# Performance work log

Measured on AMD Instinct MI355X. Metric: run time of the kernel, lower is better.

## Reference

```python
import jax, jax.numpy as jnp
import numpy as np

B, S, D, E = 4, 2048, 512, 32

def setup_inputs() -> dict:
    key = jax.random.key(0)
    k1, k2, k3 = jax.random.split(key, 3)
    x = jax.random.normal(k1, (B, S, D), dtype=jnp.float32)
    # glorot-ish scaling for weights
    gate_w = jax.random.normal(k2, (D, E), dtype=jnp.float32) * (1.0 / np.sqrt(D))
    gate_b = jnp.zeros((E,), dtype=jnp.float32)
    expert_w = jax.random.normal(k3, (E, D, D), dtype=jnp.float32) * (1.0 / np.sqrt(D))
    return {"x": x, "gate_w": gate_w, "gate_b": gate_b, "expert_w": expert_w}

def reference(x, gate_w, gate_b, expert_w):
    # gate_scores: [B,S,E] (context=None -> route on x itself)
    gate = jax.nn.softmax(jnp.einsum('bsd,de->bse', x, gate_w) + gate_b, axis=-1)
    # Dense soft-MoE: sum_e gate[b,s,e] * (x[b,s,:] @ expert_w[e])
    # Single einsum avoids materializing the [B,S,E,D] intermediate.
    out = jnp.einsum('bse,bsd,edf->bsf', gate, x, expert_w)
    return out
```

## Files before the change

### kernel.cpp

```cpp
#include <hip/hip_runtime.h>

#define TOK 8192
#define DIM 512
#define NE  32
#define KTOT (NE * DIM)

#define BM 128
#define BN 128
#define BK 64

typedef float f32x4 __attribute__((ext_vector_type(4)));
typedef short s16x8 __attribute__((ext_vector_type(8)));

typedef const void __attribute__((address_space(1)))* gp1_t;
typedef void __attribute__((address_space(3)))* lp3_t;

__device__ __forceinline__ void gl_lds16(const void* g, void* l) {
    __builtin_amdgcn_global_load_lds((gp1_t)g, (lp3_t)l, 16, 0, 0);
}

__device__ __forceinline__ ushort f2bf(float f) {
    unsigned u = __builtin_bit_cast(unsigned, f);
    unsigned r = (u + 0x7fffu + ((u >> 16) & 1u)) >> 16;
    return (ushort)r;
}

__global__ __launch_bounds__(256) void k_prep(const float* __restrict__ w,
                                              ushort* __restrict__ wt,
                                              const float* __restrict__ x,
                                              const float* __restrict__ gw,
                                              const float* __restrict__ gb,
                                              float* __restrict__ G,
                                              ushort* __restrict__ xb) {
    __shared__ __align__(16) char smem[64 * 65 * 4];
    const int bx = blockIdx.x;
    const int tid = threadIdx.x;
    if (bx < 2048) {
        float (*tile)[65] = (float(*)[65])smem;
        const int e = bx >> 6;
        const int f0 = ((bx >> 3) & 7) * 64;
        const int d0 = (bx & 7) * 64;
        const int tx = tid & 63, ty = tid >> 6;
        const float* we = w + (size_t)e * DIM * DIM;
#pragma unroll
        for (int i = ty; i < 64; i += 4)
            tile[i][tx] = we[(size_t)(d0 + i) * DIM + f0 + tx];
        __syncthreads();
#pragma unroll
        for (int i = ty; i < 64; i += 4)
            wt[(size_t)(f0 + i) * KTOT + e * DIM + d0 + tx] = f2bf(tile[tx][i]);
    } else {
        float* xs = (float*)smem;
        const int t0 = (bx - 2048) * 8;
        const float* xBase = x + (size_t)t0 * DIM;
#pragma unroll
        for (int k = 0; k < 4; ++k) {
            int i4 = (k * 256 + tid) * 4;
            float4 v = *(const float4*)(xBase + i4);
            xs[i4 + 0] = v.x; xs[i4 + 1] = v.y; xs[i4 + 2] = v.z; xs[i4 + 3] = v.w;
            ushort4 o;
            o.x = f2bf(v.x); o.y = f2bf(v.y); o.z = f2bf(v.z); o.w = f2bf(v.w);
            *(ushort4*)(xb + (size_t)t0 * DIM + i4) = o;
        }
        __syncthreads();
        const int tok = tid >> 5;
        const int e = tid & 31;
        float l = gb[e];
        const float* xr = xs + tok * DIM;
#pragma unroll 8
        for (int d = 0; d < DIM; ++d)
            l += xr[d] * gw[d * NE + e];
        float mx = l;
#pragma unroll
        for (int m = 16; m >= 1; m >>= 1) mx = fmaxf(mx, __shfl_xor(mx, m));
        float ex = expf(l - mx);
        float s = ex;
#pragma unroll
        for (int m = 16; m >= 1; m >>= 1) s += __shfl_xor(s, m);
        G[(size_t)(t0 + tok) * NE + e] = ex / s;
    }
}

__global__ __launch_bounds__(512, 2) void k_moe_gemm(const ushort* __restrict__ xb,
                                                     const ushort* __restrict__ wt,
                                                     const float* __restrict__ G,
                                                     float* __restrict__ out0,
                                                     float* __restrict__ out1) {
    __shared__ __align__(16) ushort As[2][BM * BK];
    __shared__ __align__(16) ushort Bs[2][BN * BK];
    __shared__ float Gs[16][BM];

    const int tid = threadIdx.x;
    const int m0 = blockIdx.y * BM;
    const int n0 = blockIdx.x * BN;
    const int e0 = blockIdx.z * 16;
    float* __restrict__ dst = blockIdx.z ? out1 : out0;

    for (int i = tid; i < 16 * BM; i += 512) {
        int e = i >> 7, r = i & 127;
        Gs[e][r] = G[(size_t)(m0 + r) * NE + e0 + e];
    }

    const int lane = tid & 63;
    const int wave = tid >> 6;
    const int wm = (wave & 3) * 32;
    const int wn = (wave >> 2) * 64;
    const int l15 = lane & 15;
    const int q = lane >> 4;
    const int keyR = l15 & 7;

    const int swz0 = ((q) ^ keyR) * 16;
    const int swz1 = ((4 + q) ^ keyR) * 16;
    const int rowA0 = (wm + l15) * 128;
    const int rowA1 = (wm + 16 + l15) * 128;
    const int rowB0 = (wn + l15) * 128;
    const int rowB1 = (wn + 16 + l15) * 128;
    const int rowB2 = (wn + 32 + l15) * 128;
    const int rowB3 = (wn + 48 + l15) * 128;

    const int srow = tid >> 3;
    const int chunk = tid & 7;
    const int scol = ((chunk ^ (srow & 7)) * 8);
    const ushort* aBase = xb + (size_t)(m0 + srow) * DIM + scol;
    const ushort* bBase = wt + (size_t)(n0 + srow) * KTOT + (size_t)e0 * DIM + scol;
    const int ldsOff = tid * 16;

    const f32x4 zv = {0.f, 0.f, 0.f, 0.f};
    f32x4 acc[2][4];
#pragma unroll
    for (int i = 0; i < 2; ++i)
#pragma unroll
        for (int j = 0; j < 4; ++j) acc[i][j] = zv;

    gl_lds16(aBase, (char*)As[0] + ldsOff);
    gl_lds16(aBase + (size_t)64 * DIM, (char*)As[0] + 8192 + ldsOff);
    gl_lds16(bBase, (char*)Bs[0] + ldsOff);
    gl_lds16(bBase + (size_t)64 * KTOT, (char*)Bs[0] + 8192 + ldsOff);
    __syncthreads();

#pragma unroll 1
    for (int kt = 0; kt < 8; ++kt) {
        const char* Ab = (const char*)As[kt & 1];
#pragma unroll 1
        for (int ee = 0; ee < 16; ++ee) {
            const int gn = kt * 16 + ee + 1;
            if (gn < 128) {
                const ushort* bN = bBase + (size_t)(gn & 15) * DIM + (gn >> 4) * BK;
                char* bL = (char*)Bs[gn & 1] + ldsOff;
                gl_lds16(bN, bL);
                gl_lds16(bN + (size_t)64 * KTOT, bL + 8192);
                if (ee == 15) {
                    const ushort* aN = aBase + (kt + 1) * BK;
                    char* aL = (char*)As[(kt + 1) & 1] + ldsOff;
                    gl_lds16(aN, aL);
                    gl_lds16(aN + (size_t)64 * DIM, aL + 8192);
                }
            }

            const char* Bb = (const char*)Bs[ee & 1];
            f32x4 pacc[2][4];
#pragma unroll
            for (int ks = 0; ks < 2; ++ks) {
                const int swz = ks ? swz1 : swz0;
                s16x8 a0 = *(const s16x8*)(Ab + rowA0 + swz);
                s16x8 a1 = *(const s16x8*)(Ab + rowA1 + swz);
                s16x8 b0 = *(const s16x8*)(Bb + rowB0 + swz);
                s16x8 b1 = *(const s16x8*)(Bb + rowB1 + swz);
                s16x8 b2 = *(const s16x8*)(Bb + rowB2 + swz);
                s16x8 b3 = *(const s16x8*)(Bb + rowB3 + swz);
                if (ks == 0) {
                    pacc[0][0] = __builtin_amdgcn_mfma_f32_16x16x32_bf16(a0, b0, zv, 0, 0, 0);
                    pacc[0][1] = __builtin_amdgcn_mfma_f32_16x16x32_bf16(a0, b1, zv, 0, 0, 0);
                    pacc[0][2] = __builtin_amdgcn_mfma_f32_16x16x32_bf16(a0, b2, zv, 0, 0, 0);
                    pacc[0][3] = __builtin_amdgcn_mfma_f32_16x16x32_bf16(a0, b3, zv, 0, 0, 0);
                    pacc[1][0] = __builtin_amdgcn_mfma_f32_16x16x32_bf16(a1, b0, zv, 0, 0, 0);
                    pacc[1][1] = __builtin_amdgcn_mfma_f32_16x16x32_bf16(a1, b1, zv, 0, 0, 0);
                    pacc[1][2] = __builtin_amdgcn_mfma_f32_16x16x32_bf16(a1, b2, zv, 0, 0, 0);
                    pacc[1][3] = __builtin_amdgcn_mfma_f32_16x16x32_bf16(a1, b3, zv, 0, 0, 0);
                } else {
                    pacc[0][0] = __builtin_amdgcn_mfma_f32_16x16x32_bf16(a0, b0, pacc[0][0], 0, 0, 0);
                    pacc[0][1] = __builtin_amdgcn_mfma_f32_16x16x32_bf16(a0, b1, pacc[0][1], 0, 0, 0);
                    pacc[0][2] = __builtin_amdgcn_mfma_f32_16x16x32_bf16(a0, b2, pacc[0][2], 0, 0, 0);
                    pacc[0][3] = __builtin_amdgcn_mfma_f32_16x16x32_bf16(a0, b3, pacc[0][3], 0, 0, 0);
                    pacc[1][0] = __builtin_amdgcn_mfma_f32_16x16x32_bf16(a1, b0, pacc[1][0], 0, 0, 0);
                    pacc[1][1] = __builtin_amdgcn_mfma_f32_16x16x32_bf16(a1, b1, pacc[1][1], 0, 0, 0);
                    pacc[1][2] = __builtin_amdgcn_mfma_f32_16x16x32_bf16(a1, b2, pacc[1][2], 0, 0, 0);
                    pacc[1][3] = __builtin_amdgcn_mfma_f32_16x16x32_bf16(a1, b3, pacc[1][3], 0, 0, 0);
                }
            }

#pragma unroll
            for (int i = 0; i < 2; ++i) {
                const f32x4 gt = *(const f32x4*)&Gs[ee][wm + i * 16 + q * 4];
#pragma unroll
                for (int j = 0; j < 4; ++j) {
                    acc[i][j][0] += gt[0] * pacc[i][j][0];
                    acc[i][j][1] += gt[1] * pacc[i][j][1];
                    acc[i][j][2] += gt[2] * pacc[i][j][2];
                    acc[i][j][3] += gt[3] * pacc[i][j][3];
                }
            }
            __syncthreads();
        }
    }

#pragma unroll
    for (int i = 0; i < 2; ++i) {
        const int tl = m0 + wm + i * 16 + q * 4;
#pragma unroll
        for (int j = 0; j < 4; ++j) {
            const int f = n0 + wn + j * 16 + l15;
            float* p = dst + (size_t)tl * DIM + f;
            p[0 * DIM] = acc[i][j][0];
            p[1 * DIM] = acc[i][j][1];
            p[2 * DIM] = acc[i][j][2];
            p[3 * DIM] = acc[i][j][3];
        }
    }
}

__global__ __launch_bounds__(256) void k_reduce(float* __restrict__ out,
                                                const float* __restrict__ P) {
    int i = (blockIdx.x * 256 + threadIdx.x) * 4;
    float4 a = *(const float4*)(out + i);
    float4 b = *(const float4*)(P + i);
    a.x += b.x; a.y += b.y; a.z += b.z; a.w += b.w;
    *(float4*)(out + i) = a;
}

extern "C" void kernel_launch(void* const* d_in, const int* in_sizes, int n_in,
                              void* d_out, int out_size, void* d_ws, size_t ws_size,
                              hipStream_t stream) {
    const float* x  = (const float*)d_in[0];
    const float* gw = (const float*)d_in[1];
    const float* gb = (const float*)d_in[2];
    const float* w  = (const float*)d_in[3];
    float* out = (float*)d_out;

    char* ws = (char*)d_ws;
    ushort* xb = (ushort*)ws;
    ushort* wt = (ushort*)(ws + (8u << 20));
    float*  G  = (float*)(ws + (24u << 20));
    float*  P  = (float*)(ws + (25u << 20));

    k_prep<<<dim3(2048 + TOK / 8), dim3(256), 0, stream>>>(w, wt, x, gw, gb, G, xb);
    k_moe_gemm<<<dim3(DIM / BN, TOK / BM, 2), dim3(512), 0, stream>>>(xb, wt, G, out, P);
    k_reduce<<<dim3(TOK * DIM / 1024), dim3(256), 0, stream>>>(out, P);
}
```

Measured before the change: 255.7 us.

## Hold A fragments in registers, shrink N tile, transpose gate layout

```diff
diff --git a/kernel.cpp b/kernel.cpp
--- a/kernel.cpp
+++ b/kernel.cpp
@@ -6,7 +6,7 @@
 #define KTOT (NE * DIM)
 
 #define BM 128
-#define BN 128
+#define BN 64
 #define BK 64
 
 typedef float f32x4 __attribute__((ext_vector_type(4)));
@@ -30,7 +30,7 @@
                                               const float* __restrict__ x,
                                               const float* __restrict__ gw,
                                               const float* __restrict__ gb,
-                                              float* __restrict__ G,
+                                              float* __restrict__ G2,
                                               ushort* __restrict__ xb) {
     __shared__ __align__(16) char smem[64 * 65 * 4];
     const int bx = blockIdx.x;
@@ -77,16 +77,15 @@
         float s = ex;
 #pragma unroll
         for (int m = 16; m >= 1; m >>= 1) s += __shfl_xor(s, m);
-        G[(size_t)(t0 + tok) * NE + e] = ex / s;
-    }
-}
-
-__global__ __launch_bounds__(512, 2) void k_moe_gemm(const ushort* __restrict__ xb,
+        G2[(size_t)e * TOK + t0 + tok] = ex / s;
+    }
+}
+
+__global__ __launch_bounds__(256, 4) void k_moe_gemm(const ushort* __restrict__ xb,
                                                      const ushort* __restrict__ wt,
-                                                     const float* __restrict__ G,
+                                                     const float* __restrict__ G2,
                                                      float* __restrict__ out0,
                                                      float* __restrict__ out1) {
-    __shared__ __align__(16) ushort As[2][BM * BK];
     __shared__ __align__(16) ushort Bs[2][BN * BK];
     __shared__ float Gs[16][BM];
 
@@ -96,108 +95,90 @@
     const int e0 = blockIdx.z * 16;
     float* __restrict__ dst = blockIdx.z ? out1 : out0;
 
-    for (int i = tid; i < 16 * BM; i += 512) {
+    for (int i = tid; i < 16 * BM; i += 256) {
         int e = i >> 7, r = i & 127;
-        Gs[e][r] = G[(size_t)(m0 + r) * NE + e0 + e];
+        Gs[e][r] = G2[(size_t)(e0 + e) * TOK + m0 + r];
     }
 
     const int lane = tid & 63;
     const int wave = tid >> 6;
-    const int wm = (wave & 3) * 32;
-    const int wn = (wave >> 2) * 64;
+    const int wm = (wave & 1) * 64;
+    const int wn = (wave >> 1) * 32;
     const int l15 = lane & 15;
     const int q = lane >> 4;
     const int keyR = l15 & 7;
 
-    const int swz0 = ((q) ^ keyR) * 16;
-    const int swz1 = ((4 + q) ^ keyR) * 16;
-    const int rowA0 = (wm + l15) * 128;
-    const int rowA1 = (wm + 16 + l15) * 128;
-    const int rowB0 = (wn + l15) * 128;
-    const int rowB1 = (wn + 16 + l15) * 128;
-    const int rowB2 = (wn + 32 + l15) * 128;
-    const int rowB3 = (wn + 48 + l15) * 128;
+    int rb[2][2];
+#pragma unroll
+    for (int j = 0; j < 2; ++j)
+#pragma unroll
+        for (int ks = 0; ks < 2; ++ks)
+            rb[j][ks] = (wn + j * 16 + l15) * 128 + (((ks * 4 + q) ^ keyR) << 4);
 
     const int srow = tid >> 3;
-    const int chunk = tid & 7;
-    const int scol = ((chunk ^ (srow & 7)) * 8);
-    const ushort* aBase = xb + (size_t)(m0 + srow) * DIM + scol;
+    const int c8 = tid & 7;
+    const int scol = ((c8 ^ (srow & 7)) * 8);
     const ushort* bBase = wt + (size_t)(n0 + srow) * KTOT + (size_t)e0 * DIM + scol;
+    const ushort* bBase2 = bBase + (size_t)32 * KTOT;
     const int ldsOff = tid * 16;
 
+    const ushort* aP[4];
+#pragma unroll
+    for (int i = 0; i < 4; ++i)
+        aP[i] = xb + (size_t)(m0 + wm + i * 16 + l15) * DIM + q * 8;
+
     const f32x4 zv = {0.f, 0.f, 0.f, 0.f};
-    f32x4 acc[2][4];
-#pragma unroll
-    for (int i = 0; i < 2; ++i)
-#pragma unroll
-        for (int j = 0; j < 4; ++j) acc[i][j] = zv;
-
-    gl_lds16(aBase, (char*)As[0] + ldsOff);
-    gl_lds16(aBase + (size_t)64 * DIM, (char*)As[0] + 8192 + ldsOff);
+    f32x4 acc[4][2];
+#pragma unroll
+    for (int i = 0; i < 4; ++i)
+#pragma unroll
+        for (int j = 0; j < 2; ++j) acc[i][j] = zv;
+
     gl_lds16(bBase, (char*)Bs[0] + ldsOff);
-    gl_lds16(bBase + (size_t)64 * KTOT, (char*)Bs[0] + 8192 + ldsOff);
+    gl_lds16(bBase2, (char*)Bs[0] + 4096 + ldsOff);
     __syncthreads();
 
 #pragma unroll 1
     for (int kt = 0; kt < 8; ++kt) {
-        const char* Ab = (const char*)As[kt & 1];
+        s16x8 a[4][2];
+#pragma unroll
+        for (int i = 0; i < 4; ++i) {
+            a[i][0] = *(const s16x8*)(aP[i] + kt * 64);
+            a[i][1] = *(const s16x8*)(aP[i] + kt * 64 + 32);
+        }
+
 #pragma unroll 1
         for (int ee = 0; ee < 16; ++ee) {
-            const int gn = kt * 16 + ee + 1;
-            if (gn < 128) {
+            const int g = kt * 16 + ee;
+            if (g + 1 < 128) {
+                const int gn = g + 1;
                 const ushort* bN = bBase + (size_t)(gn & 15) * DIM + (gn >> 4) * BK;
                 char* bL = (char*)Bs[gn & 1] + ldsOff;
                 gl_lds16(bN, bL);
-                gl_lds16(bN + (size_t)64 * KTOT, bL + 8192);
-                if (ee == 15) {
-                    const ushort* aN = aBase + (kt + 1) * BK;
-                    char* aL = (char*)As[(kt + 1) & 1] + ldsOff;
-                    gl_lds16(aN, aL);
-                    gl_lds16(aN + (size_t)64 * DIM, aL + 8192);
-                }
+                gl_lds16(bN + (size_t)32 * KTOT, bL + 4096);
             }
 
-            const char* Bb = (const char*)Bs[ee & 1];
-            f32x4 pacc[2][4];
-#pragma unroll
-            for (int ks = 0; ks < 2; ++ks) {
-                const int swz = ks ? swz1 : swz0;
-                s16x8 a0 = *(const s16x8*)(Ab + rowA0 + swz);
-                s16x8 a1 = *(const s16x8*)(Ab + rowA1 + swz);
-                s16x8 b0 = *(const s16x8*)(Bb + rowB0 + swz);
-                s16x8 b1 = *(const s16x8*)(Bb + rowB1 + swz);
-                s16x8 b2 = *(const s16x8*)(Bb + rowB2 + swz);
-                s16x8 b3 = *(const s16x8*)(Bb + rowB3 + swz);
-                if (ks == 0) {
-                    pacc[0][0] = __builtin_amdgcn_mfma_f32_16x16x32_bf16(a0, b0, zv, 0, 0, 0);
-                    pacc[0][1] = __builtin_amdgcn_mfma_f32_16x16x32_bf16(a0, b1, zv, 0, 0, 0);
-                    pacc[0][2] = __builtin_amdgcn_mfma_f32_16x16x32_bf16(a0, b2, zv, 0, 0, 0);
-                    pacc[0][3] = __builtin_amdgcn_mfma_f32_16x16x32_bf16(a0, b3, zv, 0, 0, 0);
-                    pacc[1][0] = __builtin_amdgcn_mfma_f32_16x16x32_bf16(a1, b0, zv, 0, 0, 0);
-                    pacc[1][1] = __builtin_amdgcn_mfma_f32_16x16x32_bf16(a1, b1, zv, 0, 0, 0);
-                    pacc[1][2] = __builtin_amdgcn_mfma_f32_16x16x32_bf16(a1, b2, zv, 0, 0, 0);
-                    pacc[1][3] = __builtin_amdgcn_mfma_f32_16x16x32_bf16(a1, b3, zv, 0, 0, 0);
-                } else {
-                    pacc[0][0] = __builtin_amdgcn_mfma_f32_16x16x32_bf16(a0, b0, pacc[0][0], 0, 0, 0);
-                    pacc[0][1] = __builtin_amdgcn_mfma_f32_16x16x32_bf16(a0, b1, pacc[0][1], 0, 0, 0);
-                    pacc[0][2] = __builtin_amdgcn_mfma_f32_16x16x32_bf16(a0, b2, pacc[0][2], 0, 0, 0);
-                    pacc[0][3] = __builtin_amdgcn_mfma_f32_16x16x32_bf16(a0, b3, pacc[0][3], 0, 0, 0);
-                    pacc[1][0] = __builtin_amdgcn_mfma_f32_16x16x32_bf16(a1, b0, pacc[1][0], 0, 0, 0);
-                    pacc[1][1] = __builtin_amdgcn_mfma_f32_16x16x32_bf16(a1, b1, pacc[1][1], 0, 0, 0);
-                    pacc[1][2] = __builtin_amdgcn_mfma_f32_16x16x32_bf16(a1, b2, pacc[1][2], 0, 0, 0);
-                    pacc[1][3] = __builtin_amdgcn_mfma_f32_16x16x32_bf16(a1, b3, pacc[1][3], 0, 0, 0);
-                }
+            const char* Bb = (const char*)Bs[g & 1];
+            s16x8 b[2][2];
+#pragma unroll
+            for (int j = 0; j < 2; ++j) {
+                b[j][0] = *(const s16x8*)(Bb + rb[j][0]);
+                b[j][1] = *(const s16x8*)(Bb + rb[j][1]);
             }
 
 #pragma unroll
-            for (int i = 0; i < 2; ++i) {
+            for (int i = 0; i < 4; ++i) {
                 const f32x4 gt = *(const f32x4*)&Gs[ee][wm + i * 16 + q * 4];
 #pragma unroll
-                for (int j = 0; j < 4; ++j) {
-                    acc[i][j][0] += gt[0] * pacc[i][j][0];
-                    acc[i][j][1] += gt[1] * pacc[i][j][1];
-                    acc[i][j][2] += gt[2] * pacc[i][j][2];
-                    acc[i][j][3] += gt[3] * pacc[i][j][3];
+                for (int j = 0; j < 2; ++j) {
+                    f32x4 p = __builtin_amdgcn_mfma_f32_16x16x32_bf16(
+                        a[i][0], b[j][0], zv, 0, 0, 0);
+                    p = __builtin_amdgcn_mfma_f32_16x16x32_bf16(
+                        a[i][1], b[j][1], p, 0, 0, 0);
+                    acc[i][j][0] += gt[0] * p[0];
+                    acc[i][j][1] += gt[1] * p[1];
+                    acc[i][j][2] += gt[2] * p[2];
+                    acc[i][j][3] += gt[3] * p[3];
                 }
             }
             __syncthreads();
@@ -205,10 +186,10 @@
     }
 
 #pragma unroll
-    for (int i = 0; i < 2; ++i) {
+    for (int i = 0; i < 4; ++i) {
         const int tl = m0 + wm + i * 16 + q * 4;
 #pragma unroll
-        for (int j = 0; j < 4; ++j) {
+        for (int j = 0; j < 2; ++j) {
             const int f = n0 + wn + j * 16 + l15;
             float* p = dst + (size_t)tl * DIM + f;
             p[0 * DIM] = acc[i][j][0];
@@ -240,10 +221,10 @@
     char* ws = (char*)d_ws;
     ushort* xb = (ushort*)ws;
     ushort* wt = (ushort*)(ws + (8u << 20));
-    float*  G  = (float*)(ws + (24u << 20));
+    float*  G2 = (float*)(ws + (24u << 20));
     float*  P  = (float*)(ws + (25u << 20));
 
-    k_prep<<<dim3(2048 + TOK / 8), dim3(256), 0, stream>>>(w, wt, x, gw, gb, G, xb);
-    k_moe_gemm<<<dim3(DIM / BN, TOK / BM, 2), dim3(512), 0, stream>>>(xb, wt, G, out, P);
+    k_prep<<<dim3(2048 + TOK / 8), dim3(256), 0, stream>>>(w, wt, x, gw, gb, G2, xb);
+    k_moe_gemm<<<dim3(DIM / BN, TOK / BM, 2), dim3(256), 0, stream>>>(xb, wt, G2, out, P);
     k_reduce<<<dim3(TOK * DIM / 1024), dim3(256), 0, stream>>>(out, P);
 }
```

After: 273.2 us. 6.8% more time.
